# Performance work log

Measured on AMD Instinct MI355X. Metric: run time of the kernel, lower is better.

The kernel has to match this reference:

```python
import jax, jax.numpy as jnp
import numpy as np

S = 14
L_COORD = 5.0
L_NOOBJ = 0.5


def setup_inputs() -> dict:
    key = jax.random.key(0)
    k1, k2, k3 = jax.random.split(key, 3)
    B = 4096
    pred = jax.random.uniform(k1, (B, S, S, 30), dtype=jnp.float32)
    target = jax.random.uniform(k2, (B, S, S, 30), dtype=jnp.float32)
    # matching real YOLO targets where most cells are background.
    gate = jax.random.uniform(k3, (B, S, S))
    conf = jnp.where(gate > 0.85, target[..., 4], 0.0)
    target = target.at[..., 4].set(conf)
    return {"pred_tensor": pred, "target_tensor": target}


def _to_xyxy(b):
    # b: (..., 5) [x, y, w, h, c] -> (..., 4) [x1, y1, x2, y2]
    c = b[..., :2] / 14.0
    half = 0.5 * b[..., 2:4]
    return jnp.concatenate([c - half, c + half], axis=-1)


def _iou_2v1(pbox, tbox):
    # pbox: (B,S,S,2,4) xyxy, tbox: (B,S,S,4) -> iou (B,S,S,2)
    lt = jnp.maximum(pbox[..., :2], tbox[..., None, :2])
    rb = jnp.minimum(pbox[..., 2:], tbox[..., None, 2:])
    wh = jnp.clip(rb - lt, 0.0)
    inter = wh[..., 0] * wh[..., 1]
    a1 = (pbox[..., 2] - pbox[..., 0]) * (pbox[..., 3] - pbox[..., 1])
    a2 = (tbox[..., 2] - tbox[..., 0]) * (tbox[..., 3] - tbox[..., 1])
    return inter / (a1 + a2[..., None] - inter)


def reference(pred_tensor, target_tensor):
    pred, target = pred_tensor, target_tensor
    N = pred.shape[0]
    dt = pred.dtype
    coo = (target[..., 4] > 0).astype(dt)          # (B,S,S) object cells
    noo = 1.0 - coo                                # background cells

    # no-object confidence loss over both conf slots (indices 4 and 9)
    noobj_loss = jnp.sum(noo * ((pred[..., 4] - target[..., 4]) ** 2
                                + (pred[..., 9] - target[..., 9]) ** 2))

    # boxes: (B,S,S,2,5)
    pb = pred[..., :10].reshape(pred.shape[0], S, S, 2, 5)
    tb = target[..., :10].reshape(target.shape[0], S, S, 2, 5)

    # IoU of both predicted boxes vs first target box; detached (torch uses .data)
    iou = jax.lax.stop_gradient(_iou_2v1(_to_xyxy(pb), _to_xyxy(tb[..., 0, :])))
    resp = jax.nn.one_hot(jnp.argmax(iou, axis=-1), 2, dtype=dt)  # (B,S,S,2)
    max_iou = jnp.max(iou, axis=-1)                               # (B,S,S)

    p_resp = jnp.einsum('bijk,bijkc->bijc', resp, pb)  # responsible pred box
    t_resp = jnp.einsum('bijk,bijkc->bijc', resp, tb)  # matching target box
    conf_not_resp = jnp.einsum('bijk,bijk->bij', 1.0 - resp, pb[..., 4])

    contain_loss = jnp.sum(coo * (p_resp[..., 4] - max_iou) ** 2)
    not_contain_loss = jnp.sum(coo * conf_not_resp ** 2)  # target conf forced to 0

    loc_loss = jnp.sum(coo[..., None] * ((p_resp[..., :2] - t_resp[..., :2]) ** 2
               + (jnp.sqrt(p_resp[..., 2:4]) - jnp.sqrt(t_resp[..., 2:4])) ** 2))

    class_loss = jnp.sum(coo[..., None] * (pred[..., 10:] - target[..., 10:]) ** 2)

    total = (L_COORD * loc_loss + contain_loss
             + L_NOOBJ * (noobj_loss + not_contain_loss) + class_loss) / N
    return total
```

## Files before the change

kernel.cpp:

```cpp
#include <hip/hip_runtime.h>


#define CPW 64
#define F4P 480
#define F4C (2 * F4P)
#define LPI 15
#define NBLOCKS 2560

__device__ __forceinline__ void gload_lds16(const void* g, void* s) {
    auto g1 = (const __attribute__((address_space(1))) void*)(uintptr_t)g;
    auto s3 = (__attribute__((address_space(3))) void*)(uint32_t)(uintptr_t)s;
    __builtin_amdgcn_global_load_lds(g1, s3, 16, 0, 0);
}

__device__ __forceinline__ float cell_loss(const float* __restrict__ p,
                                           const float* __restrict__ t)
{
    const bool coo = t[4] > 0.0f;
    if (!coo) {
        float d4 = p[4] - t[4];
        float d9 = p[9] - t[9];
        return 0.5f * (d4 * d4 + d9 * d9);
    }
    const float inv14 = 1.0f / 14.0f;
    float p0x1 = p[0]*inv14 - 0.5f*p[2], p0y1 = p[1]*inv14 - 0.5f*p[3];
    float p0x2 = p[0]*inv14 + 0.5f*p[2], p0y2 = p[1]*inv14 + 0.5f*p[3];
    float p1x1 = p[5]*inv14 - 0.5f*p[7], p1y1 = p[6]*inv14 - 0.5f*p[8];
    float p1x2 = p[5]*inv14 + 0.5f*p[7], p1y2 = p[6]*inv14 + 0.5f*p[8];
    float tx1  = t[0]*inv14 - 0.5f*t[2], ty1  = t[1]*inv14 - 0.5f*t[3];
    float tx2  = t[0]*inv14 + 0.5f*t[2], ty2  = t[1]*inv14 + 0.5f*t[3];

    float at = (tx2 - tx1) * (ty2 - ty1);

    float w0 = fmaxf(fminf(p0x2, tx2) - fmaxf(p0x1, tx1), 0.0f);
    float h0 = fmaxf(fminf(p0y2, ty2) - fmaxf(p0y1, ty1), 0.0f);
    float inter0 = w0 * h0;
    float a0 = (p0x2 - p0x1) * (p0y2 - p0y1);
    float iou0 = inter0 / (a0 + at - inter0);

    float w1 = fmaxf(fminf(p1x2, tx2) - fmaxf(p1x1, tx1), 0.0f);
    float h1 = fmaxf(fminf(p1y2, ty2) - fmaxf(p1y1, ty1), 0.0f);
    float inter1 = w1 * h1;
    float a1 = (p1x2 - p1x1) * (p1y2 - p1y1);
    float iou1 = inter1 / (a1 + at - inter1);

    bool  r1      = iou1 > iou0;
    float max_iou = fmaxf(iou0, iou1);

    float prx = r1 ? p[5] : p[0], pry = r1 ? p[6] : p[1];
    float prw = r1 ? p[7] : p[2], prh = r1 ? p[8] : p[3];
    float prc = r1 ? p[9] : p[4];
    float trx = r1 ? t[5] : t[0], try_ = r1 ? t[6] : t[1];
    float trw = r1 ? t[7] : t[2], trh = r1 ? t[8] : t[3];
    float cnr = r1 ? p[4] : p[9];

    float dc = prc - max_iou;
    float contain = dc * dc;
    float not_contain = cnr * cnr;

    float dx = prx - trx, dy = pry - try_;
    float dw = sqrtf(prw) - sqrtf(trw);
    float dh = sqrtf(prh) - sqrtf(trh);
    float loc = dx * dx + dy * dy + dw * dw + dh * dh;

    float cls = 0.0f;
#pragma unroll
    for (int k = 10; k < 30; ++k) {
        float d = p[k] - t[k];
        cls += d * d;
    }
    return 5.0f * loc + contain + 0.5f * not_contain + cls;
}

__global__ __launch_bounds__(64) void yolo_cells(
    const float* __restrict__ pred, const float* __restrict__ targ,
    float* __restrict__ partial, int ncells)
{
    __shared__ float4 smem4[F4C];
    const float4* P4 = reinterpret_cast<const float4*>(pred);
    const float4* T4 = reinterpret_cast<const float4*>(targ);

    const int  lane   = threadIdx.x;
    const int  wtiles = (ncells + CPW - 1) / CPW;
    const long maxf4  = (long)ncells * 30 / 4 - 1;

    float acc = 0.0f;

    for (int tile = blockIdx.x; tile < wtiles; tile += gridDim.x) {
#pragma unroll
        for (int i = 0; i < LPI; ++i) {
            int  j   = i * 64 + lane;
            bool isP = j < F4P;
            long g   = (long)tile * F4P + (isP ? j : j - F4P);
            if (g > maxf4) g = maxf4;
            gload_lds16(isP ? (const void*)(P4 + g) : (const void*)(T4 + g),
                        (void*)&smem4[i * 64]);
        }
        asm volatile("s_waitcnt vmcnt(0)" ::: "memory");
        __builtin_amdgcn_sched_barrier(0);

        const float* base = reinterpret_cast<const float*>(&smem4[0]);
        int cell = tile * CPW + lane;
        if (cell < ncells)
            acc += cell_loss(base + lane * 30, base + F4P * 4 + lane * 30);
    }

#pragma unroll
    for (int off = 32; off > 0; off >>= 1)
        acc += __shfl_down(acc, off, 64);
    if (lane == 0) partial[blockIdx.x] = acc;
}

__global__ __launch_bounds__(256) void yolo_final(
    const float* __restrict__ partial, int n, float* __restrict__ out, float invN)
{
    __shared__ float sm[256];
    float acc = 0.0f;
    for (int i = threadIdx.x; i < n; i += 256) acc += partial[i];
    sm[threadIdx.x] = acc;
    __syncthreads();
#pragma unroll
    for (int s = 128; s > 0; s >>= 1) {
        if (threadIdx.x < s) sm[threadIdx.x] += sm[threadIdx.x + s];
        __syncthreads();
    }
    if (threadIdx.x == 0) out[0] = sm[0] * invN;
}

extern "C" void kernel_launch(void* const* d_in, const int* in_sizes, int n_in,
                              void* d_out, int out_size, void* d_ws, size_t ws_size,
                              hipStream_t stream) {
    const float* pred = (const float*)d_in[0];
    const float* targ = (const float*)d_in[1];
    float* out = (float*)d_out;
    float* partial = (float*)d_ws;

    const int ncells = in_sizes[0] / 30;
    const int B      = ncells / 196;
    const float invN = 1.0f / (float)B;

    const int wtiles  = (ncells + CPW - 1) / CPW;
    const int nblocks = wtiles < NBLOCKS ? wtiles : NBLOCKS;

    yolo_cells<<<nblocks, 64, 0, stream>>>(pred, targ, partial, ncells);
    yolo_final<<<1, 256, 0, stream>>>(partial, nblocks, out, invN);
}
```

Baseline: 37.97 us.

## Prefetch next tile into registers while computing current tile from LDS

Replaces the direct global-to-LDS async loads with register loads, and software-pipelines the tile loop so the next tile's 15 float4 loads are issued before computing the current tile. The registers are then written into LDS after compute. The goal is to hide global memory latency behind the per-cell loss computation. In exchange it raises register pressure by 60 VGPRs per thread. With a single wave per block there are no barriers, and the LDS overwrite after compute relies on wave-synchronous execution.

```diff
diff --git a/kernel.cpp b/kernel.cpp
--- a/kernel.cpp
+++ b/kernel.cpp
@@ -6,12 +6,6 @@
 #define F4C (2 * F4P)
 #define LPI 15
 #define NBLOCKS 2560
-
-__device__ __forceinline__ void gload_lds16(const void* g, void* s) {
-    auto g1 = (const __attribute__((address_space(1))) void*)(uintptr_t)g;
-    auto s3 = (__attribute__((address_space(3))) void*)(uint32_t)(uintptr_t)s;
-    __builtin_amdgcn_global_load_lds(g1, s3, 16, 0, 0);
-}
 
 __device__ __forceinline__ float cell_loss(const float* __restrict__ p,
                                            const float* __restrict__ t)
@@ -85,24 +79,46 @@
     const long maxf4  = (long)ncells * 30 / 4 - 1;
 
     float acc = 0.0f;
+    float4 r[LPI];
+    int tile = blockIdx.x;
 
-    for (int tile = blockIdx.x; tile < wtiles; tile += gridDim.x) {
+    if (tile < wtiles) {
 #pragma unroll
         for (int i = 0; i < LPI; ++i) {
             int  j   = i * 64 + lane;
             bool isP = j < F4P;
             long g   = (long)tile * F4P + (isP ? j : j - F4P);
             if (g > maxf4) g = maxf4;
-            gload_lds16(isP ? (const void*)(P4 + g) : (const void*)(T4 + g),
-                        (void*)&smem4[i * 64]);
+            r[i] = isP ? P4[g] : T4[g];
         }
-        asm volatile("s_waitcnt vmcnt(0)" ::: "memory");
+#pragma unroll
+        for (int i = 0; i < LPI; ++i) smem4[i * 64 + lane] = r[i];
+    }
+
+    for (; tile < wtiles; tile += gridDim.x) {
+        int next = tile + gridDim.x;
+        bool have_next = next < wtiles;
+        if (have_next) {
+#pragma unroll
+            for (int i = 0; i < LPI; ++i) {
+                int  j   = i * 64 + lane;
+                bool isP = j < F4P;
+                long g   = (long)next * F4P + (isP ? j : j - F4P);
+                if (g > maxf4) g = maxf4;
+                r[i] = isP ? P4[g] : T4[g];
+            }
+        }
         __builtin_amdgcn_sched_barrier(0);
 
         const float* base = reinterpret_cast<const float*>(&smem4[0]);
         int cell = tile * CPW + lane;
         if (cell < ncells)
             acc += cell_loss(base + lane * 30, base + F4P * 4 + lane * 30);
+
+        if (have_next) {
+#pragma unroll
+            for (int i = 0; i < LPI; ++i) smem4[i * 64 + lane] = r[i];
+        }
     }
 
 #pragma unroll
```

Result: slower. 91.69 us (+141.5%).
